# Kernel tuning notes

Measured on AMD Instinct MI355X. Metric: run time of the kernel, lower is better.

## Reference

```python
import jax, jax.numpy as jnp
import numpy as np

SIZE = 64
B, NMAX = 8, 24


def setup_inputs() -> dict:
    key = jax.random.key(0)
    ks = jax.random.split(key, 8)
    # valid boxes: top-left in [0,400), width/height in [10,210)
    xy = jax.random.uniform(ks[0], (B, NMAX, 2)) * 400.0
    wh = jax.random.uniform(ks[1], (B, NMAX, 2)) * 200.0 + 10.0
    bboxes = jnp.concatenate([xy, xy + wh], axis=-1)  # [B,N,4] (x1,y1,x2,y2)
    num_obj = jax.random.randint(ks[2], (B,), 2, NMAX + 1)
    conv1_w = jax.random.normal(ks[3], (64, 2, 5, 5)) * 0.1
    conv1_b = jnp.zeros((64,), jnp.float32)
    conv2_w = jax.random.normal(ks[4], (32, 64, 5, 5)) * 0.05
    conv2_b = jnp.zeros((32,), jnp.float32)
    lin_w = jax.random.normal(ks[5], (5408, 4800)) * 0.01
    lin_b = jnp.zeros((4800,), jnp.float32)
    return dict(bboxes=bboxes, num_obj=num_obj, conv1_w=conv1_w, conv1_b=conv1_b,
                conv2_w=conv2_w, conv2_b=conv2_b, lin_w=lin_w, lin_b=lin_b)


def _pair_indices(num_obj):
    # ragged pair construction on host; num_obj is an integer constant input
    n = np.asarray(num_obj)
    bs, is_, js = [], [], []
    for b in range(n.shape[0]):
        ii, jj = np.triu_indices(int(n[b]), k=1)
        bs.append(np.full(ii.shape, b, dtype=np.int32))
        is_.append(ii.astype(np.int32))
        js.append(jj.astype(np.int32))
    return np.concatenate(bs), np.concatenate(is_), np.concatenate(js)


def _get_sp(boxA, boxB):
    # DRG-style spatial map: rescale both boxes into the union-box frame
    # (aspect preserving, shorter axis centered), rasterize as binary masks.
    # boxA, boxB: [M,4] -> [M,2,64,64]
    u1 = jnp.minimum(boxA[:, 0], boxB[:, 0])
    v1 = jnp.minimum(boxA[:, 1], boxB[:, 1])
    u2 = jnp.maximum(boxA[:, 2], boxB[:, 2])
    v2 = jnp.maximum(boxA[:, 3], boxB[:, 3])
    w = u2 - u1
    h = v2 - v1
    scale = (SIZE - 1.0) / jnp.maximum(jnp.maximum(w, h), 1e-6)
    offx = jnp.where(h >= w, (SIZE - 1.0 - w * scale) * 0.5, 0.0)
    offy = jnp.where(w > h, (SIZE - 1.0 - h * scale) * 0.5, 0.0)

    xs = jnp.arange(SIZE, dtype=jnp.float32)[None, None, :]
    ys = jnp.arange(SIZE, dtype=jnp.float32)[None, :, None]

    def rast(box):
        x1 = jnp.round((box[:, 0] - u1) * scale + offx)[:, None, None]
        y1 = jnp.round((box[:, 1] - v1) * scale + offy)[:, None, None]
        x2 = jnp.round((box[:, 2] - u1) * scale + offx)[:, None, None]
        y2 = jnp.round((box[:, 3] - v1) * scale + offy)[:, None, None]
        m = (xs >= x1) & (xs <= x2) & (ys >= y1) & (ys <= y2)
        return m.astype(jnp.float32)

    return jnp.stack([rast(boxA), rast(boxB)], axis=1)


def _conv(x, w, b):
    y = jax.lax.conv_general_dilated(x, w, (1, 1), 'VALID',
                                     dimension_numbers=('NCHW', 'OIHW', 'NCHW'))
    return y + b[None, :, None, None]


def _pool(x):
    return jax.lax.reduce_window(x, -jnp.inf, jax.lax.max,
                                 (1, 1, 2, 2), (1, 1, 2, 2), 'VALID')


def reference(bboxes, num_obj, conv1_w, conv1_b, conv2_w, conv2_b, lin_w, lin_b):
    bi, ii, ji = _pair_indices(num_obj)
    boxA = bboxes[bi, ii]                       # [M,4]
    boxB = bboxes[bi, ji]                       # [M,4]
    sp = _get_sp(boxA, boxB)                    # [M,2,64,64]
    x = jax.nn.relu(_conv(sp, conv1_w, conv1_b))   # [M,64,60,60]
    x = _pool(x)                                   # [M,64,30,30]
    x = jax.nn.relu(_conv(x, conv2_w, conv2_b))    # [M,32,26,26]
    x = _pool(x)                                   # [M,32,13,13]
    x = x.reshape(x.shape[0], -1)                  # [M,5408]
    feat = jax.nn.relu(x @ lin_w + lin_b)          # [M,4800]
    slicing = jnp.stack([jnp.asarray(bi), jnp.asarray(ii), jnp.asarray(ji)],
                        axis=1).astype(jnp.float32)  # [M,3]
    return feat, slicing
```

## Files before the change

### kernel.cpp

```cpp
#include <hip/hip_runtime.h>
#include <hip/hip_bf16.h>

typedef __attribute__((ext_vector_type(8))) short short8;
typedef __attribute__((ext_vector_type(4))) float f32x4;

__device__ inline unsigned short f2bf(float x) {
  unsigned u = __float_as_uint(x);
  unsigned rounding = 0x7FFFu + ((u >> 16) & 1u);
  return (unsigned short)((u + rounding) >> 16);
}
__device__ inline float bf2f(unsigned short u) {
  return __uint_as_float(((unsigned)u) << 16);
}
__device__ inline void gload_lds16(const void* g, void* l) {
  __builtin_amdgcn_global_load_lds(
      (const __attribute__((address_space(1))) unsigned int*)g,
      (__attribute__((address_space(3))) unsigned int*)l, 16, 0, 0);
}

__global__ void prep_pairs(const float* __restrict__ bboxes,
                           const int* __restrict__ num_obj, int M,
                           int* __restrict__ pairTab,
                           float* __restrict__ slicing) {
  __shared__ int cum[9];
  if (threadIdx.x == 0) {
    int c = 0; cum[0] = 0;
    for (int b = 0; b < 8; b++) { int n = num_obj[b]; c += n*(n-1)/2; cum[b+1] = c; }
  }
  __syncthreads();
  for (int m = threadIdx.x; m < M; m += blockDim.x) {
    int b = 0;
    while (b < 7 && m >= cum[b+1]) b++;
    int p = m - cum[b];
    int n = num_obj[b];
    int i = 0, rem = p;
    while (rem >= (n - 1 - i)) { rem -= (n - 1 - i); i++; }
    int j = i + 1 + rem;
    const float* A = bboxes + (b*24 + i)*4;
    const float* Bb = bboxes + (b*24 + j)*4;
    float ax1=A[0], ay1=A[1], ax2=A[2], ay2=A[3];
    float bx1=Bb[0], by1=Bb[1], bx2=Bb[2], by2=Bb[3];
    float u1 = fminf(ax1,bx1), v1 = fminf(ay1,by1);
    float u2 = fmaxf(ax2,bx2), v2 = fmaxf(ay2,by2);
    float w = u2-u1, h = v2-v1;
    float scale = 63.0f / fmaxf(fmaxf(w,h), 1e-6f);
    float offx = (h >= w) ? __fmul_rn(63.0f - __fmul_rn(w,scale), 0.5f) : 0.0f;
    float offy = (w > h)  ? __fmul_rn(63.0f - __fmul_rn(h,scale), 0.5f) : 0.0f;
    int* t = pairTab + m*8;
    t[0] = (int)rintf(__fadd_rn(__fmul_rn(ax1-u1, scale), offx));
    t[1] = (int)rintf(__fadd_rn(__fmul_rn(ay1-v1, scale), offy));
    t[2] = (int)rintf(__fadd_rn(__fmul_rn(ax2-u1, scale), offx));
    t[3] = (int)rintf(__fadd_rn(__fmul_rn(ay2-v1, scale), offy));
    t[4] = (int)rintf(__fadd_rn(__fmul_rn(bx1-u1, scale), offx));
    t[5] = (int)rintf(__fadd_rn(__fmul_rn(by1-v1, scale), offy));
    t[6] = (int)rintf(__fadd_rn(__fmul_rn(bx2-u1, scale), offx));
    t[7] = (int)rintf(__fadd_rn(__fmul_rn(by2-v1, scale), offy));
    slicing[m*3+0] = (float)b;
    slicing[m*3+1] = (float)i;
    slicing[m*3+2] = (float)j;
  }
}

__global__ void prep_tables(const float* __restrict__ w1, const float* __restrict__ w2,
                            float* __restrict__ T, unsigned short* __restrict__ W2A) {
  int idx = blockIdx.x*256 + threadIdx.x;
  if (idx < 86528) {
    int o = idx & 63;
    int t = idx >> 6;
    int rxi = t % 26; t /= 26;
    int ryi = t % 26;
    int c = t / 26;
    int ky0 = ryi/5, ky1 = ryi%5, kx0 = rxi/5, kx1 = rxi%5;
    float s = 0.f;
    for (int ky = ky0; ky <= ky1; ky++)
      for (int kx = kx0; kx <= kx1; kx++)
        s += w1[((o*2 + c)*5 + ky)*5 + kx];
    T[idx] = s;
  } else if (idx < 86528 + 51200) {
    int i = idx - 86528;
    int j = i & 7, ln = (i>>3) & 63;
    int mtk = i >> 9;
    int mt = mtk & 1, kk = mtk >> 1;
    int oc = mt*16 + (ln & 15);
    int k = kk*32 + ((ln>>4)<<3) + j;
    int halfk = k/800, r = k%800;
    int kyx = r >> 5, icl = r & 31;
    int ic = halfk*32 + icl, ky = kyx/5, kx = kyx%5;
    W2A[i] = f2bf(w2[((oc*64 + ic)*5 + ky)*5 + kx]);
  }
}

__global__ __launch_bounds__(256) void prep_wt(const float* __restrict__ lw,
                                               unsigned short* __restrict__ Wt) {
  __shared__ unsigned short tile[64][65];
  int k0 = blockIdx.x*64, n0 = blockIdx.y*64;
  for (int i = threadIdx.x; i < 64*64; i += 256) {
    int r = i >> 6, cdx = i & 63;
    int k = k0 + r, n = n0 + cdx;
    float v = (k < 5408) ? lw[(size_t)k*4800 + n] : 0.f;
    tile[r][cdx] = f2bf(v);
  }
  __syncthreads();
  for (int i = threadIdx.x; i < 64*64; i += 256) {
    int r = i >> 6, cdx = i & 63;
    int n = n0 + r, k = k0 + cdx;
    if (k < 5408) Wt[(size_t)n*5408 + k] = tile[cdx][r];
  }
}

__global__ __launch_bounds__(256) void pair_conv(
    const int* __restrict__ pairTab, const float* __restrict__ T,
    const unsigned short* __restrict__ W2A, const float* __restrict__ b1,
    const float* __restrict__ b2, unsigned short* __restrict__ X) {
  __shared__ unsigned short p1[28800];
  __shared__ unsigned char rIdx[4][64];
  int m = blockIdx.x;
  int tid = threadIdx.x, lane = tid & 63, wid = tid >> 6;
  const int* pt = pairTab + m*8;

  if (tid < 240) {
    int q = tid % 60, which = tid / 60;
    int lo, hi;
    if (which == 0)      { lo = pt[1]; hi = pt[3]; }
    else if (which == 1) { lo = pt[5]; hi = pt[7]; }
    else if (which == 2) { lo = pt[0]; hi = pt[2]; }
    else                 { lo = pt[4]; hi = pt[6]; }
    int k0 = lo - q; if (k0 < 0) k0 = 0;
    int k1 = hi - q; if (k1 > 4) k1 = 4;
    rIdx[which][q] = (k0 > k1) ? (unsigned char)25 : (unsigned char)(k0*5 + k1);
  }

  int rowbase[11];
#pragma unroll
  for (int tt = 0; tt < 11; tt++) {
    int pos = (wid*11 + tt)*16 + (lane & 15);
    if (pos > 675) pos = 675;
    rowbase[tt] = (pos/26)*30 + (pos % 26);
  }
  f32x4 acc[11][2];
#pragma unroll
  for (int tt = 0; tt < 11; tt++) {
    acc[tt][0] = (f32x4){0.f,0.f,0.f,0.f};
    acc[tt][1] = (f32x4){0.f,0.f,0.f,0.f};
  }

  int icgl = lane >> 4;
  for (int half = 0; half < 2; half++) {
    __syncthreads();
    for (int item = tid; item < 3600; item += 256) {
      int pos = item >> 2;
      int icg = item & 3;
      int ic0 = half*32 + icg*8;
      int py = pos / 30, px = pos % 30;
      float best[8];
#pragma unroll
      for (int j = 0; j < 8; j++) best[j] = -1e30f;
#pragma unroll
      for (int d = 0; d < 4; d++) {
        int y = py*2 + (d>>1), x = px*2 + (d&1);
        int rya = rIdx[0][y], ryb = rIdx[1][y];
        int rxa = rIdx[2][x], rxb = rIdx[3][x];
        const float* Ta = T + (((rya)*26 + rxa)<<6) + ic0;
        const float* Tb = T + (((26 + ryb)*26 + rxb)<<6) + ic0;
        f32x4 a0 = *(const f32x4*)Ta, a1 = *(const f32x4*)(Ta+4);
        f32x4 c0 = *(const f32x4*)Tb, c1 = *(const f32x4*)(Tb+4);
#pragma unroll
        for (int j = 0; j < 4; j++) {
          best[j]   = fmaxf(best[j],   a0[j]+c0[j]);
          best[4+j] = fmaxf(best[4+j], a1[j]+c1[j]);
        }
      }
      short8 v;
#pragma unroll
      for (int j = 0; j < 8; j++)
        v[j] = (short)f2bf(fmaxf(best[j] + b1[ic0+j], 0.f));
      int byte = pos*64 + ((icg ^ ((pos>>1)&3))<<4);
      *(short8*)((char*)p1 + byte) = v;
    }
    __syncthreads();
    for (int kl = 0; kl < 25; kl++) {
      int kk = half*25 + kl;
      const unsigned short* wptr = W2A + ((size_t)(kk*2)*64 + lane)*8;
      short8 a0 = *(const short8*)wptr;
      short8 a1 = *(const short8*)(wptr + 512);
      int radd = (kl/5)*30 + (kl%5);
#pragma unroll
      for (int tt = 0; tt < 11; tt++) {
        int row = rowbase[tt] + radd;
        int byte = row*64 + ((icgl ^ ((row>>1)&3))<<4);
        short8 bv = *(const short8*)((const char*)p1 + byte);
        acc[tt][0] = __builtin_amdgcn_mfma_f32_16x16x32_bf16(a0, bv, acc[tt][0], 0, 0, 0);
        acc[tt][1] = __builtin_amdgcn_mfma_f32_16x16x32_bf16(a1, bv, acc[tt][1], 0, 0, 0);
      }
    }
  }
  __syncthreads();
#pragma unroll
  for (int tt = 0; tt < 11; tt++) {
    int pos = (wid*11 + tt)*16 + (lane & 15);
    if (pos <= 675) {
#pragma unroll
      for (int mt = 0; mt < 2; mt++)
#pragma unroll
        for (int r = 0; r < 4; r++) {
          int oc = mt*16 + ((lane>>4)<<2) + r;
          p1[oc*676 + pos] = f2bf(acc[tt][mt][r]);
        }
    }
  }
  __syncthreads();
  for (int f = tid; f < 5408; f += 256) {
    int oc = f / 169, rem = f % 169;
    int py = rem / 13, px = rem % 13;
    const unsigned short* c2 = p1 + oc*676 + py*52 + px*2;
    float v = fmaxf(fmaxf(bf2f(c2[0]), bf2f(c2[1])), fmaxf(bf2f(c2[26]), bf2f(c2[27])));
    X[(size_t)m*5408 + f] = f2bf(fmaxf(v + b2[oc], 0.f));
  }
}

__global__ __launch_bounds__(256) void gemm_lin(
    const unsigned short* __restrict__ X, const unsigned short* __restrict__ Wt,
    const float* __restrict__ lin_b, float* __restrict__ out, int M) {
  __shared__ unsigned short As[4096], Bs[4096];
  int tid = threadIdx.x, lane = tid & 63, wid = tid >> 6;
  int m0 = blockIdx.x * 128, n0 = blockIdx.y * 128;
  int wm = wid >> 1, wn = wid & 1;
  f32x4 acc[4][4];
#pragma unroll
  for (int i = 0; i < 4; i++)
#pragma unroll
    for (int j = 0; j < 4; j++) acc[i][j] = (f32x4){0.f,0.f,0.f,0.f};

  int rA[2], kcA[2];
#pragma unroll
  for (int cc = 0; cc < 2; cc++) {
    int chunk = wid + cc*4;
    int r = (chunk<<4) + (lane>>2);
    rA[cc] = r;
    kcA[cc] = (lane&3) ^ ((r>>1)&3);
  }
  int kg = lane >> 4;

  for (int k0 = 0; k0 < 5408; k0 += 32) {
    __syncthreads();
#pragma unroll
    for (int cc = 0; cc < 2; cc++) {
      int chunk = wid + cc*4;
      int r = rA[cc], kc = kcA[cc];
      int gm = m0 + r; if (gm > M-1) gm = M-1;
      int gn = n0 + r; if (gn > 4799) gn = 4799;
      gload_lds16(X  + (size_t)gm*5408 + k0 + kc*8, (char*)As + chunk*1024);
      gload_lds16(Wt + (size_t)gn*5408 + k0 + kc*8, (char*)Bs + chunk*1024);
    }
    __syncthreads();
    short8 af[4], bfr[4];
#pragma unroll
    for (int mf = 0; mf < 4; mf++) {
      int row = wm*64 + mf*16 + (lane&15);
      int byte = row*64 + ((kg ^ ((row>>1)&3))<<4);
      af[mf] = *(const short8*)((const char*)As + byte);
    }
#pragma unroll
    for (int nf = 0; nf < 4; nf++) {
      int row = wn*64 + nf*16 + (lane&15);
      int byte = row*64 + ((kg ^ ((row>>1)&3))<<4);
      bfr[nf] = *(const short8*)((const char*)Bs + byte);
    }
#pragma unroll
    for (int mf = 0; mf < 4; mf++)
#pragma unroll
      for (int nf = 0; nf < 4; nf++)
        acc[mf][nf] = __builtin_amdgcn_mfma_f32_16x16x32_bf16(af[mf], bfr[nf], acc[mf][nf], 0, 0, 0);
  }

#pragma unroll
  for (int mf = 0; mf < 4; mf++) {
#pragma unroll
    for (int nf = 0; nf < 4; nf++) {
      int n = n0 + wn*64 + nf*16 + (lane&15);
#pragma unroll
      for (int r = 0; r < 4; r++) {
        int mm = m0 + wm*64 + mf*16 + ((lane>>4)<<2) + r;
        if (mm < M && n < 4800)
          out[(size_t)mm*4800 + n] = fmaxf(acc[mf][nf][r] + lin_b[n], 0.f);
      }
    }
  }
}

extern "C" void kernel_launch(void* const* d_in, const int* in_sizes, int n_in,
                              void* d_out, int out_size, void* d_ws, size_t ws_size,
                              hipStream_t stream) {
  const float* bboxes = (const float*)d_in[0];
  const int*   num_obj = (const int*)d_in[1];
  const float* w1 = (const float*)d_in[2];
  const float* b1 = (const float*)d_in[3];
  const float* w2 = (const float*)d_in[4];
  const float* b2 = (const float*)d_in[5];
  const float* lw = (const float*)d_in[6];
  const float* lb = (const float*)d_in[7];
  float* out = (float*)d_out;
  int M = out_size / 4803;

  char* ws = (char*)d_ws;
  size_t off = 0;
  auto alloc = [&](size_t bytes) {
    off = (off + 511) & ~(size_t)511;
    char* p = ws + off;
    off += bytes;
    return p;
  };
  int* pairTab = (int*)alloc((size_t)M*8*4);
  float* T = (float*)alloc((size_t)86528*4);
  unsigned short* W2A = (unsigned short*)alloc((size_t)51200*2);
  unsigned short* Wt = (unsigned short*)alloc((size_t)4800*5408*2);
  unsigned short* X = (unsigned short*)alloc((size_t)M*5408*2);

  prep_pairs<<<1, 256, 0, stream>>>(bboxes, num_obj, M, pairTab, out + (size_t)M*4800);
  prep_tables<<<(137728+255)/256, 256, 0, stream>>>(w1, w2, T, W2A);
  prep_wt<<<dim3(85, 75), 256, 0, stream>>>(lw, Wt);
  pair_conv<<<M, 256, 0, stream>>>(pairTab, T, W2A, b1, b2, X);
  gemm_lin<<<dim3((M+127)/128, 38), 256, 0, stream>>>(X, Wt, lb, out, M);
}
```

Baseline: 318.2 us.

## Add split-K with double-buffered 64-wide K tiles to the linear GEMM

Pads the K dimension of the transposed weights and activations to 5440 so the GEMM can stage 64-wide K tiles with no bounds checks. The GEMM now uses 64x128 output tiles, double-buffers its LDS loads to overlap the global-to-LDS copy with the MFMA work, and splits K across up to four blocks in grid z. That multiplies the number of blocks, which were too few to fill the device. Partial sums go to an fp32 workspace, and a separate reduce kernel applies bias and ReLU. In exchange it adds extra global traffic for the partials and an extra launch.

```diff
diff --git a/kernel.cpp b/kernel.cpp
--- a/kernel.cpp
+++ b/kernel.cpp
@@ -17,6 +17,9 @@
       (const __attribute__((address_space(1))) unsigned int*)g,
       (__attribute__((address_space(3))) unsigned int*)l, 16, 0, 0);
 }
+
+#define KPAD 5440
+#define NPAD 4864
 
 __global__ void prep_pairs(const float* __restrict__ bboxes,
                            const int* __restrict__ num_obj, int M,
@@ -104,7 +107,7 @@
   for (int i = threadIdx.x; i < 64*64; i += 256) {
     int r = i >> 6, cdx = i & 63;
     int n = n0 + r, k = k0 + cdx;
-    if (k < 5408) Wt[(size_t)n*5408 + k] = tile[cdx][r];
+    Wt[(size_t)n*KPAD + k] = tile[cdx][r];
   }
 }
 
@@ -209,82 +212,129 @@
     }
   }
   __syncthreads();
-  for (int f = tid; f < 5408; f += 256) {
-    int oc = f / 169, rem = f % 169;
-    int py = rem / 13, px = rem % 13;
-    const unsigned short* c2 = p1 + oc*676 + py*52 + px*2;
-    float v = fmaxf(fmaxf(bf2f(c2[0]), bf2f(c2[1])), fmaxf(bf2f(c2[26]), bf2f(c2[27])));
-    X[(size_t)m*5408 + f] = f2bf(fmaxf(v + b2[oc], 0.f));
+  for (int f = tid; f < KPAD; f += 256) {
+    unsigned short outv = 0;
+    if (f < 5408) {
+      int oc = f / 169, rem = f % 169;
+      int py = rem / 13, px = rem % 13;
+      const unsigned short* c2 = p1 + oc*676 + py*52 + px*2;
+      float v = fmaxf(fmaxf(bf2f(c2[0]), bf2f(c2[1])), fmaxf(bf2f(c2[26]), bf2f(c2[27])));
+      outv = f2bf(fmaxf(v + b2[oc], 0.f));
+    }
+    X[(size_t)m*KPAD + f] = outv;
   }
 }
 
 __global__ __launch_bounds__(256) void gemm_lin(
     const unsigned short* __restrict__ X, const unsigned short* __restrict__ Wt,
-    const float* __restrict__ lin_b, float* __restrict__ out, int M) {
-  __shared__ unsigned short As[4096], Bs[4096];
+    const float* __restrict__ lin_b, float* __restrict__ P, float* __restrict__ out,
+    int M, int Mpad, int splits) {
+  __shared__ unsigned short As[2][4096];
+  __shared__ unsigned short Bs[2][8192];
   int tid = threadIdx.x, lane = tid & 63, wid = tid >> 6;
-  int m0 = blockIdx.x * 128, n0 = blockIdx.y * 128;
+  int m0 = blockIdx.x * 64, n0 = blockIdx.y * 128;
+  int ks = blockIdx.z;
+  int itBeg = (ks * 85) / splits, itEnd = ((ks + 1) * 85) / splits;
   int wm = wid >> 1, wn = wid & 1;
-  f32x4 acc[4][4];
-#pragma unroll
-  for (int i = 0; i < 4; i++)
+
+  f32x4 acc[2][4];
+#pragma unroll
+  for (int i = 0; i < 2; i++)
 #pragma unroll
     for (int j = 0; j < 4; j++) acc[i][j] = (f32x4){0.f,0.f,0.f,0.f};
 
-  int rA[2], kcA[2];
-#pragma unroll
-  for (int cc = 0; cc < 2; cc++) {
-    int chunk = wid + cc*4;
-    int r = (chunk<<4) + (lane>>2);
-    rA[cc] = r;
-    kcA[cc] = (lane&3) ^ ((r>>1)&3);
-  }
+  int rsub = lane >> 3;
+  int kslot = (lane & 7) ^ rsub;
   int kg = lane >> 4;
 
-  for (int k0 = 0; k0 < 5408; k0 += 32) {
-    __syncthreads();
+  auto stage = [&](int buf, int it) {
+    size_t kof = (size_t)it * 64 + kslot * 8;
 #pragma unroll
     for (int cc = 0; cc < 2; cc++) {
       int chunk = wid + cc*4;
-      int r = rA[cc], kc = kcA[cc];
-      int gm = m0 + r; if (gm > M-1) gm = M-1;
-      int gn = n0 + r; if (gn > 4799) gn = 4799;
-      gload_lds16(X  + (size_t)gm*5408 + k0 + kc*8, (char*)As + chunk*1024);
-      gload_lds16(Wt + (size_t)gn*5408 + k0 + kc*8, (char*)Bs + chunk*1024);
+      int gm = m0 + chunk*8 + rsub;
+      gload_lds16(X + (size_t)gm*KPAD + kof, (char*)As[buf] + chunk*1024);
+    }
+#pragma unroll
+    for (int cc = 0; cc < 4; cc++) {
+      int chunk = wid + cc*4;
+      int gn = n0 + chunk*8 + rsub;
+      gload_lds16(Wt + (size_t)gn*KPAD + kof, (char*)Bs[buf] + chunk*1024);
+    }
+  };
+
+  stage(0, itBeg);
+  __syncthreads();
+  int cur = 0;
+  for (int it = itBeg; it < itEnd; ++it) {
+    if (it + 1 < itEnd) stage(cur ^ 1, it + 1);
+#pragma unroll
+    for (int ksub = 0; ksub < 2; ++ksub) {
+      int slot = ksub*4 + kg;
+      short8 af[2], bfr[4];
+#pragma unroll
+      for (int mf = 0; mf < 2; mf++) {
+        int r = wm*32 + mf*16 + (lane & 15);
+        af[mf] = *(const short8*)((const char*)As[cur] + r*128 + ((slot ^ (lane&7))<<4));
+      }
+#pragma unroll
+      for (int nf = 0; nf < 4; nf++) {
+        int r = wn*64 + nf*16 + (lane & 15);
+        bfr[nf] = *(const short8*)((const char*)Bs[cur] + r*128 + ((slot ^ (lane&7))<<4));
+      }
+#pragma unroll
+      for (int mf = 0; mf < 2; mf++)
+#pragma unroll
+        for (int nf = 0; nf < 4; nf++)
+          acc[mf][nf] = __builtin_amdgcn_mfma_f32_16x16x32_bf16(af[mf], bfr[nf], acc[mf][nf], 0, 0, 0);
     }
     __syncthreads();
-    short8 af[4], bfr[4];
-#pragma unroll
-    for (int mf = 0; mf < 4; mf++) {
-      int row = wm*64 + mf*16 + (lane&15);
-      int byte = row*64 + ((kg ^ ((row>>1)&3))<<4);
-      af[mf] = *(const short8*)((const char*)As + byte);
-    }
-#pragma unroll
-    for (int nf = 0; nf < 4; nf++) {
-      int row = wn*64 + nf*16 + (lane&15);
-      int byte = row*64 + ((kg ^ ((row>>1)&3))<<4);
-      bfr[nf] = *(const short8*)((const char*)Bs + byte);
-    }
-#pragma unroll
-    for (int mf = 0; mf < 4; mf++)
-#pragma unroll
-      for (int nf = 0; nf < 4; nf++)
-        acc[mf][nf] = __builtin_amdgcn_mfma_f32_16x16x32_bf16(af[mf], bfr[nf], acc[mf][nf], 0, 0, 0);
-  }
-
-#pragma unroll
-  for (int mf = 0; mf < 4; mf++) {
-#pragma unroll
-    for (int nf = 0; nf < 4; nf++) {
-      int n = n0 + wn*64 + nf*16 + (lane&15);
-#pragma unroll
-      for (int r = 0; r < 4; r++) {
-        int mm = m0 + wm*64 + mf*16 + ((lane>>4)<<2) + r;
-        if (mm < M && n < 4800)
-          out[(size_t)mm*4800 + n] = fmaxf(acc[mf][nf][r] + lin_b[n], 0.f);
-      }
-    }
+    cur ^= 1;
+  }
+
+  if (splits == 1) {
+#pragma unroll
+    for (int mf = 0; mf < 2; mf++)
+#pragma unroll
+      for (int nf = 0; nf < 4; nf++) {
+        int n = n0 + wn*64 + nf*16 + (lane & 15);
+#pragma unroll
+        for (int r = 0; r < 4; r++) {
+          int mm = m0 + wm*32 + mf*16 + ((lane>>4)<<2) + r;
+          if (mm < M && n < 4800)
+            out[(size_t)mm*4800 + n] = fmaxf(acc[mf][nf][r] + lin_b[n], 0.f);
+        }
+      }
+  } else {
+    float* Pp = P + (size_t)ks * Mpad * NPAD;
+#pragma unroll
+    for (int mf = 0; mf < 2; mf++)
+#pragma unroll
+      for (int nf = 0; nf < 4; nf++) {
+        int n = n0 + wn*64 + nf*16 + (lane & 15);
+#pragma unroll
+        for (int r = 0; r < 4; r++) {
+          int mm = m0 + wm*32 + mf*16 + ((lane>>4)<<2) + r;
+          Pp[(size_t)mm*NPAD + n] = acc[mf][nf][r];
+        }
+      }
+  }
+}
+
+__global__ void reduce_out(const float* __restrict__ P, const float* __restrict__ lb,
+                           float* __restrict__ out, int M, int Mpad, int splits) {
+  int total = M * 1200;
+  for (int idx = blockIdx.x*256 + threadIdx.x; idx < total; idx += gridDim.x*256) {
+    int m = idx / 1200, q = idx - m*1200;
+    int n = q * 4;
+    f32x4 s = *(const f32x4*)(P + (size_t)m*NPAD + n);
+    for (int sidx = 1; sidx < splits; sidx++)
+      s += *(const f32x4*)(P + (size_t)sidx*Mpad*NPAD + (size_t)m*NPAD + n);
+    f32x4 b = *(const f32x4*)(lb + n);
+    f32x4 r;
+#pragma unroll
+    for (int j = 0; j < 4; j++) r[j] = fmaxf(s[j] + b[j], 0.f);
+    *(f32x4*)(out + (size_t)m*4800 + n) = r;
   }
 }
 
@@ -301,11 +351,22 @@
   const float* lb = (const float*)d_in[7];
   float* out = (float*)d_out;
   int M = out_size / 4803;
+  int Mpad = (M + 63) & ~63;
+
+  size_t fixed = 0;
+  auto align512 = [](size_t x) { return (x + 511) & ~(size_t)511; };
+  fixed += align512((size_t)M*8*4);
+  fixed += align512((size_t)86528*4);
+  fixed += align512((size_t)51200*2);
+  fixed += align512((size_t)4800*KPAD*2);
+  fixed += align512((size_t)Mpad*KPAD*2);
+  int splits = 4;
+  while (splits > 1 && fixed + align512((size_t)splits*Mpad*NPAD*4) > ws_size) splits >>= 1;
 
   char* ws = (char*)d_ws;
   size_t off = 0;
   auto alloc = [&](size_t bytes) {
-    off = (off + 511) & ~(size_t)511;
+    off = align512(off);
     char* p = ws + off;
     off += bytes;
     return p;
@@ -313,12 +374,15 @@
   int* pairTab = (int*)alloc((size_t)M*8*4);
   float* T = (float*)alloc((size_t)86528*4);
   unsigned short* W2A = (unsigned short*)alloc((size_t)51200*2);
-  unsigned short* Wt = (unsigned short*)alloc((size_t)4800*5408*2);
-  unsigned short* X = (unsigned short*)alloc((size_t)M*5408*2);
+  unsigned short* Wt = (unsigned short*)alloc((size_t)4800*KPAD*2);
+  unsigned short* X = (unsigned short*)alloc((size_t)Mpad*KPAD*2);
+  float* P = (splits > 1) ? (float*)alloc((size_t)splits*Mpad*NPAD*4) : nullptr;
 
   prep_pairs<<<1, 256, 0, stream>>>(bboxes, num_obj, M, pairTab, out + (size_t)M*4800);
   prep_tables<<<(137728+255)/256, 256, 0, stream>>>(w1, w2, T, W2A);
   prep_wt<<<dim3(85, 75), 256, 0, stream>>>(lw, Wt);
   pair_conv<<<M, 256, 0, stream>>>(pairTab, T, W2A, b1, b2, X);
-  gemm_lin<<<dim3((M+127)/128, 38), 256, 0, stream>>>(X, Wt, lb, out, M);
-}
+  gemm_lin<<<dim3(Mpad/64, 38, splits), 256, 0, stream>>>(X, Wt, lb, P, out, M, Mpad, splits);
+  if (splits > 1)
+    reduce_out<<<1024, 256, 0, stream>>>(P, lb, out, M, Mpad, splits);
+}
```

Result: faster. 278.7 us (-12.4%).
